# Kernel optimization log

Hardware: AMD Instinct MI355X
Metric: run time of the kernel (lower is better)

The kernel has to match this reference:

```python
import jax, jax.numpy as jnp
import numpy as np

DEMO_T = 4
N_HEADS = 4
N_LAYERS = 2
EPS = 1e-5
IN_DIM = 512
FF_DIM = 128
TEMP = float(np.sqrt(IN_DIM))  # temperature=None -> sqrt(in_dim)


def setup_inputs() -> dict:
    key = jax.random.key(0)
    ks = jax.random.split(key, 12)
    B, d, T, H, W = 8, IN_DIM, 36, 7, 12
    s_in = 1.0 / np.sqrt(d)
    s_ff = 1.0 / np.sqrt(FF_DIM)
    f32 = jnp.float32
    return {
        "inputs": jax.random.normal(ks[0], (B, d, T, H, W), f32),
        "demo_wq": jax.random.normal(ks[1], (N_LAYERS, FF_DIM, d), f32) * s_in,
        "demo_wk": jax.random.normal(ks[2], (N_LAYERS, FF_DIM, d), f32) * s_in,
        "demo_wv": jax.random.normal(ks[3], (N_LAYERS, FF_DIM, d), f32) * s_in,
        "demo_wo": jax.random.normal(ks[4], (N_LAYERS, d, FF_DIM), f32) * s_ff,
        "obs_wq": jax.random.normal(ks[5], (N_LAYERS, FF_DIM, d), f32) * s_in,
        "obs_wk": jax.random.normal(ks[6], (N_LAYERS, FF_DIM, d), f32) * s_in,
        "obs_wv": jax.random.normal(ks[7], (N_LAYERS, FF_DIM, d), f32) * s_in,
        "obs_wo": jax.random.normal(ks[8], (N_LAYERS, d, FF_DIM), f32) * s_ff,
        "bn_gamma": jnp.ones((N_LAYERS, d), f32),
        "bn_beta": jnp.zeros((N_LAYERS, d), f32),
    }


def _conv1x1(w, x):
    # 1x1x1 Conv3d, bias=False == per-voxel channel mixing
    return jnp.einsum('od,bdthw->bothw', w, x)


def _forward(inputs, demo_wq, demo_wk, demo_wv, demo_wo,
             obs_wq, obs_wk, obs_wv, obs_wo, bn_gamma, bn_beta):
    B, d, T, H, W = inputs.shape
    HW = H * W
    obs_T = T - DEMO_T
    neg_inf = jnp.asarray(-jnp.inf, inputs.dtype)
    # causal log-mask over demo tokens, block-expanded to spatial positions
    tril = jnp.tril(jnp.ones((DEMO_T, DEMO_T), inputs.dtype))
    mask = jnp.repeat(jnp.repeat(tril, HW, axis=0), HW, axis=1)  # (dTHW, dTHW)
    log_mask = jnp.where(mask > 0, jnp.asarray(0.0, inputs.dtype), neg_inf)

    x = inputs
    for i in range(N_LAYERS):
        demo_in = x[:, :, :DEMO_T]   # [B,d,dT,H,W]
        obs_in = x[:, :, DEMO_T:]    # [B,d,oT,H,W]

        # --- demo self-attention (causal) ---
        def demo_heads(w):
            y = _conv1x1(w, demo_in)                      # [B,ff,dT,H,W]
            return y.reshape(B, N_HEADS, -1, DEMO_T * HW)  # [B,n,ch,dTHW]
        dq, dk, dv = demo_heads(demo_wq[i]), demo_heads(demo_wk[i]), demo_heads(demo_wv[i])
        dkq = jnp.einsum('bnci,bncj->bnij', dk, dq) / TEMP + log_mask
        dattn = jax.nn.softmax(dkq, axis=-1)               # softmax over j (as in source)
        dv_att = jnp.einsum('bncj,bnij->bnci', dv, dattn)  # attended demo values
        # NOTE: the source computes demo_out via demo_Outs + relu-skip but never
        # uses it downstream (dead code); only dv_att/dk feed the obs fusion.

        # --- obs attention, fused with demo keys/attended-values ---
        def obs_heads(w):
            y = _conv1x1(w, obs_in)                        # [B,ff,oT,H,W]
            y = y.reshape(B, N_HEADS, -1, obs_T, HW)
            return jnp.transpose(y, (0, 3, 1, 2, 4))       # [B,oT,n,ch,HW]
        oq, ok, ov = obs_heads(obs_wq[i]), obs_heads(obs_wk[i]), obs_heads(obs_wv[i])
        rep_k = jnp.broadcast_to(dk[:, None], (B, obs_T) + dk.shape[1:])
        rep_v = jnp.broadcast_to(dv_att[:, None], (B, obs_T) + dv_att.shape[1:])
        cat_k = jnp.concatenate([rep_k, ok], axis=-1)      # [B,oT,n,ch,(1+dT)HW]
        cat_v = jnp.concatenate([rep_v, ov], axis=-1)
        okq = jnp.einsum('btnci,btncj->btnij', cat_k, oq) / TEMP  # i=cat len, j=HW
        oattn = jax.nn.softmax(okq, axis=-1)               # softmax over j (source: dim=4)
        ov_att = jnp.einsum('btncj,btnji->btnci', cat_v, oattn)  # [B,oT,n,ch,HW]
        obs_out = _conv1x1(obs_wo[i],
                           jnp.transpose(ov_att, (0, 2, 3, 1, 4)).reshape(B, -1, obs_T, H, W))
        # skip (out_dim == in_dim), dropout=0 -> identity
        obs_res = obs_in + jax.nn.relu(obs_out)

        # shared BatchNorm3d (training-mode batch stats) over concatenated streams
        x = jnp.concatenate([demo_in, obs_res], axis=2)
        mean = x.mean(axis=(0, 2, 3, 4)).reshape(1, -1, 1, 1, 1)
        var = x.var(axis=(0, 2, 3, 4)).reshape(1, -1, 1, 1, 1)
        g = bn_gamma[i].reshape(1, -1, 1, 1, 1)
        b = bn_beta[i].reshape(1, -1, 1, 1, 1)
        x = g * (x - mean) * jax.lax.rsqrt(var + EPS) + b
    return x  # == out_dict['last']


def reference(inputs, demo_wq, demo_wk, demo_wv, demo_wo,
              obs_wq, obs_wk, obs_wv, obs_wo, bn_gamma, bn_beta):
    return _forward(inputs, demo_wq, demo_wk, demo_wv, demo_wo,
                    obs_wq, obs_wk, obs_wv, obs_wo, bn_gamma, bn_beta)
```

## Files before the change

kernel.cpp:

```cpp
#include <hip/hip_runtime.h>

#define B_N 8
#define D_N 512
#define T_N 36
#define HW_N 84
#define THW_N 3024
#define DT_N 4
#define OT_N 32
#define NH_N 4
#define FF_N 128
#define CH_N 32
#define DI_N 336
#define OI_N 2688
#define CAT_N 420
#define INV_TEMP 0.04419417382415922f
#define BN_EPS 1e-5f
#define INV_CNT (1.0f / 24192.0f)

#define SW_DWQ 0
#define SW_DWK 131072
#define SW_DWV 262144
#define SW_OWQ 393216
#define SW_OWK 524288
#define SW_OWV 655360
#define SW_OWO 786432
#define S_DQ   917504
#define S_DK   1261568
#define S_DV   1605632
#define S_DVA  1949696
#define S_OQ   2293760
#define S_OK   5046272
#define S_OV   7798784
#define S_OVA  10551296
#define S_XBF  13303808

typedef short bf16x8 __attribute__((ext_vector_type(8)));
typedef float f32x4 __attribute__((ext_vector_type(4)));

__device__ __forceinline__ short f2bf(float f) {
    unsigned u = __float_as_uint(f);
    u += 0x7fffu + ((u >> 16) & 1u);
    return (short)(u >> 16);
}
__device__ __forceinline__ float bf2f(short s) {
    return __uint_as_float(((unsigned)(unsigned short)s) << 16);
}

__global__ __launch_bounds__(256) void cvt_w_kernel(
    const float* __restrict__ s0, const float* __restrict__ s1,
    const float* __restrict__ s2, const float* __restrict__ s3,
    const float* __restrict__ s4, const float* __restrict__ s5,
    const float* __restrict__ s6, short* __restrict__ dst,
    float* __restrict__ stats)
{
    const int bid = blockIdx.x;
    if (bid == 0) {
        #pragma unroll
        for (int k = 0; k < 8; ++k) stats[threadIdx.x * 8 + k] = 0.f;
    }
    const int a = bid >> 6, blk = bid & 63;
    const float* src;
    switch (a) {
        case 0: src = s0; break; case 1: src = s1; break;
        case 2: src = s2; break; case 3: src = s3; break;
        case 4: src = s4; break; case 5: src = s5; break;
        default: src = s6;
    }
    const int idx = (blk * 256 + (int)threadIdx.x) * 8;
    float4 f0 = *reinterpret_cast<const float4*>(src + idx);
    float4 f1 = *reinterpret_cast<const float4*>(src + idx + 4);
    bf16x8 pk;
    pk[0] = f2bf(f0.x); pk[1] = f2bf(f0.y); pk[2] = f2bf(f0.z); pk[3] = f2bf(f0.w);
    pk[4] = f2bf(f1.x); pk[5] = f2bf(f1.y); pk[6] = f2bf(f1.z); pk[7] = f2bf(f1.w);
    *reinterpret_cast<bf16x8*>(dst + (size_t)a * 131072 + idx) = pk;
}

__global__ __launch_bounds__(256) void xin_kernel(
    const float* __restrict__ in_f, short* __restrict__ xbf,
    float* __restrict__ stats0)
{
    __shared__ short tile[48][65];
    __shared__ float red_s[16][64];
    __shared__ float red_q[16][64];

    const int bid = blockIdx.x;
    const int b = bid / 504, rem = bid % 504, tt = rem >> 3, cblk = rem & 7;
    const int t0 = tt * 48, c0 = cblk * 64;
    const int tid = threadIdx.x;
    const bool is_demo = (tt < 7);

    #pragma unroll
    for (int l0 = 0; l0 < 768; l0 += 256) {
        int l = l0 + tid;
        int cc = l / 12, tg = l % 12;
        size_t addr = ((size_t)b * D_N + c0 + cc) * THW_N + t0 + tg * 4;
        float4 v = *reinterpret_cast<const float4*>(in_f + addr);
        tile[tg * 4 + 0][cc] = f2bf(v.x);
        tile[tg * 4 + 1][cc] = f2bf(v.y);
        tile[tg * 4 + 2][cc] = f2bf(v.z);
        tile[tg * 4 + 3][cc] = f2bf(v.w);
    }
    __syncthreads();
    float psum[4] = {}, psq[4] = {};
    const int cg = tid & 15;
    #pragma unroll
    for (int l0 = 0; l0 < 768; l0 += 256) {
        int l = l0 + tid;
        int tk = l >> 4;
        short4 s4;
        s4.x = tile[tk][cg * 4 + 0];
        s4.y = tile[tk][cg * 4 + 1];
        s4.z = tile[tk][cg * 4 + 2];
        s4.w = tile[tk][cg * 4 + 3];
        *reinterpret_cast<short4*>(
            xbf + ((size_t)b * THW_N + t0 + tk) * 512 + c0 + cg * 4) = s4;
        if (is_demo) {
            float v0 = bf2f(s4.x), v1 = bf2f(s4.y), v2 = bf2f(s4.z), v3 = bf2f(s4.w);
            psum[0] += v0; psum[1] += v1; psum[2] += v2; psum[3] += v3;
            psq[0] += v0 * v0; psq[1] += v1 * v1; psq[2] += v2 * v2; psq[3] += v3 * v3;
        }
    }
    if (!is_demo) return;
    __syncthreads();
    #pragma unroll
    for (int j = 0; j < 4; ++j) {
        red_s[tid >> 4][cg * 4 + j] = psum[j];
        red_q[tid >> 4][cg * 4 + j] = psq[j];
    }
    __syncthreads();
    if (tid < 64) {
        float s = 0.f, q = 0.f;
        #pragma unroll
        for (int r = 0; r < 16; ++r) { s += red_s[r][tid]; q += red_q[r][tid]; }
        atomicAdd(&stats0[c0 + tid], s);
        atomicAdd(&stats0[512 + c0 + tid], q);
    }
}

__global__ __launch_bounds__(256) void proj_mfma_kernel(
    const short* __restrict__ xbf, short* __restrict__ ws, int layer)
{
    __shared__ short As[3][4096];
    __shared__ short Bs[1536];

    const int bid = blockIdx.x;
    const int b = bid / 63, ct = bid - b * 63;
    const bool is_demo = (ct < 7);
    const int woff = layer * 65536;
    const short* W0 = ws + (is_demo ? SW_DWQ : SW_OWQ) + woff;
    const short* W1 = ws + (is_demo ? SW_DWK : SW_OWK) + woff;
    const short* W2 = ws + (is_demo ? SW_DWV : SW_OWV) + woff;
    const int Ltok = is_demo ? DI_N : OI_N;
    const int colL = is_demo ? ct * 48 : (ct - 7) * 48;
    short* Yq = ws + (is_demo ? S_DQ : S_OQ);
    short* Yk = ws + (is_demo ? S_DK : S_OK);
    short* Yv = ws + (is_demo ? S_DV : S_OV);
    const short* Xb = xbf + ((size_t)b * THW_N + (is_demo ? 0 : DI_N) + colL) * 512;

    const int tid = threadIdx.x;
    const int lane = tid & 63, wv = tid >> 6;
    const int l15 = lane & 15, q = lane >> 4;

    f32x4 acc[3][2][3] = {};

    for (int k0 = 0; k0 < D_N; k0 += 32) {
        __syncthreads();
        const short* Wt[3] = {W0, W1, W2};
        #pragma unroll
        for (int wt = 0; wt < 3; ++wt) {
            #pragma unroll
            for (int h = 0; h < 2; ++h) {
                int c = tid + h * 256;
                int kc = c & 3, m = c >> 2;
                bf16x8 pk = *reinterpret_cast<const bf16x8*>(
                    Wt[wt] + (size_t)m * D_N + k0 + kc * 8);
                *reinterpret_cast<bf16x8*>(&As[wt][(kc * 128 + m) * 8]) = pk;
            }
        }
        if (tid < 192) {
            int n = tid % 48, kc = tid / 48;
            bf16x8 pk = *reinterpret_cast<const bf16x8*>(
                Xb + (size_t)n * 512 + k0 + kc * 8);
            *reinterpret_cast<bf16x8*>(&Bs[(kc * 48 + n) * 8]) = pk;
        }
        __syncthreads();

        bf16x8 bfr[3];
        #pragma unroll
        for (int nt = 0; nt < 3; ++nt)
            bfr[nt] = *reinterpret_cast<const bf16x8*>(&Bs[(q * 48 + nt * 16 + l15) * 8]);
        #pragma unroll
        for (int wt = 0; wt < 3; ++wt) {
            #pragma unroll
            for (int mt2 = 0; mt2 < 2; ++mt2) {
                bf16x8 afr = *reinterpret_cast<const bf16x8*>(
                    &As[wt][(q * 128 + wv * 32 + mt2 * 16 + l15) * 8]);
                #pragma unroll
                for (int nt = 0; nt < 3; ++nt)
                    acc[wt][mt2][nt] = __builtin_amdgcn_mfma_f32_16x16x32_bf16(
                        afr, bfr[nt], acc[wt][mt2][nt], 0, 0, 0);
            }
        }
    }

    #pragma unroll
    for (int mt2 = 0; mt2 < 2; ++mt2) {
        int mrow = wv * 32 + mt2 * 16 + q * 4;
        #pragma unroll
        for (int nt = 0; nt < 3; ++nt) {
            int token = colL + nt * 16 + l15;
            f32x4 aq = acc[0][mt2][nt] * INV_TEMP;
            short4 s4;
            s4.x = f2bf(aq[0]); s4.y = f2bf(aq[1]); s4.z = f2bf(aq[2]); s4.w = f2bf(aq[3]);
            *reinterpret_cast<short4*>(Yq + ((size_t)b * Ltok + token) * 128 + mrow) = s4;
            f32x4 ak = acc[1][mt2][nt];
            s4.x = f2bf(ak[0]); s4.y = f2bf(ak[1]); s4.z = f2bf(ak[2]); s4.w = f2bf(ak[3]);
            *reinterpret_cast<short4*>(Yk + ((size_t)b * Ltok + token) * 128 + mrow) = s4;
            #pragma unroll
            for (int r = 0; r < 4; ++r)
                Yv[((size_t)b * FF_N + mrow + r) * Ltok + token] = f2bf(acc[2][mt2][nt][r]);
        }
    }
}

template<int NT>
__device__ __forceinline__ void demo_core(
    const short* __restrict__ dqS, const short* __restrict__ dkS,
    const short* __restrict__ dvS, short* __restrict__ dvaS,
    short* __restrict__ Pt, int b, int n, int ti, int ih)
{
    constexpr int NTP = (NT + 1) & ~1;
    const int tid = threadIdx.x;
    const int lane = tid & 63, w = tid >> 6;
    const int l15 = lane & 15, q = lane >> 4;
    const int jmax = (ti + 1) * 84;

    const int irow = ih * 48 + w * 16 + l15;
    const int tokA = ti * 84 + (irow < 84 ? irow : 83);
    bf16x8 afr = *reinterpret_cast<const bf16x8*>(
        dkS + ((size_t)b * DI_N + tokA) * 128 + n * 32 + q * 8);

    f32x4 s[NT];
    #pragma unroll
    for (int nt = 0; nt < NT; ++nt) {
        bf16x8 bfr = *reinterpret_cast<const bf16x8*>(
            dqS + ((size_t)b * DI_N + nt * 16 + l15) * 128 + n * 32 + q * 8);
        f32x4 z = {};
        s[nt] = __builtin_amdgcn_mfma_f32_16x16x32_bf16(afr, bfr, z, 0, 0, 0);
    }

    const int mstart = jmax - (NT - 1) * 16;
    #pragma unroll
    for (int r = 0; r < 4; ++r) {
        if (l15 >= mstart) s[NT - 1][r] = -3.0e38f;
        float mx = s[0][r];
        #pragma unroll
        for (int nt = 1; nt < NT; ++nt) mx = fmaxf(mx, s[nt][r]);
        #pragma unroll
        for (int o = 1; o < 16; o <<= 1) mx = fmaxf(mx, __shfl_xor(mx, o));
        float sm = 0.f;
        #pragma unroll
        for (int nt = 0; nt < NT; ++nt) {
            float e = __expf(s[nt][r] - mx);
            s[nt][r] = e; sm += e;
        }
        #pragma unroll
        for (int o = 1; o < 16; o <<= 1) sm += __shfl_xor(sm, o);
        float inv = 1.f / sm;
        #pragma unroll
        for (int nt = 0; nt < NT; ++nt) s[nt][r] *= inv;
    }

    #pragma unroll
    for (int nt = 0; nt < NT; ++nt)
        #pragma unroll
        for (int r = 0; r < 4; ++r)
            Pt[(w * 16 + q * 4 + r) * 360 + nt * 16 + l15] = f2bf(s[nt][r]);
    if (NTP != NT) {
        #pragma unroll
        for (int r = 0; r < 4; ++r)
            Pt[(w * 16 + q * 4 + r) * 360 + NT * 16 + l15] = 0;
    }
    __syncthreads();

    f32x4 oacc[2] = {};
    #pragma unroll
    for (int kk = 0; kk < NTP / 2; ++kk) {
        bf16x8 pb = *reinterpret_cast<const bf16x8*>(
            &Pt[(w * 16 + l15) * 360 + kk * 32 + q * 8]);
        #pragma unroll
        for (int ct = 0; ct < 2; ++ct) {
            bf16x8 va = *reinterpret_cast<const bf16x8*>(
                dvS + ((size_t)b * FF_N + n * 32 + ct * 16 + l15) * DI_N + kk * 32 + q * 8);
            oacc[ct] = __builtin_amdgcn_mfma_f32_16x16x32_bf16(va, pb, oacc[ct], 0, 0, 0);
        }
    }

    const int ig = ih * 48 + w * 16 + l15;
    if (ig < 84) {
        #pragma unroll
        for (int ct = 0; ct < 2; ++ct)
            #pragma unroll
            for (int r = 0; r < 4; ++r)
                dvaS[((size_t)b * FF_N + n * 32 + ct * 16 + q * 4 + r) * DI_N + ti * 84 + ig] =
                    f2bf(oacc[ct][r]);
    }
}

__global__ __launch_bounds__(192) void demo_attn_mfma_kernel(const short* __restrict__ ws)
{
    __shared__ short Pt[48 * 360];

    const short* dqS = ws + S_DQ;
    const short* dkS = ws + S_DK;
    const short* dvS = ws + S_DV;
    short* dvaS = const_cast<short*>(ws) + S_DVA;

    const int bid = blockIdx.x;
    const int ih = bid & 1, ti = (bid >> 1) & 3;
    const int n = (bid >> 3) & 3, b = bid >> 5;

    switch (ti) {
        case 0: demo_core<6>(dqS, dkS, dvS, dvaS, Pt, b, n, ti, ih); break;
        case 1: demo_core<11>(dqS, dkS, dvS, dvaS, Pt, b, n, ti, ih); break;
        case 2: demo_core<16>(dqS, dkS, dvS, dvaS, Pt, b, n, ti, ih); break;
        default: demo_core<21>(dqS, dkS, dvS, dvaS, Pt, b, n, ti, ih); break;
    }
}

__global__ __launch_bounds__(256, 4) void obs_attn_mfma_kernel(const short* __restrict__ ws)
{
    __shared__ short Qt[96 * 40];
    __shared__ short Kt[64 * 40];
    __shared__ short Vs[32 * 72];
    __shared__ short Pt[96 * 72];

    const short* dkS = ws + S_DK;
    const short* dvaS = ws + S_DVA;
    const short* oqS = ws + S_OQ;
    const short* okS = ws + S_OK;
    const short* ovS = ws + S_OV;
    short* ovaS = const_cast<short*>(ws) + S_OVA;

    const int bid = blockIdx.x;
    const int b = bid >> 7, rem = bid & 127, t = rem >> 2, n = rem & 3;

    const int tid = threadIdx.x;
    const int lane = tid & 63, wv = tid >> 6;
    const int l15 = lane & 15, q = lane >> 4;

    for (int l = tid; l < 384; l += 256) {
        int i = l >> 2, c0 = (l & 3) * 8;
        bf16x8 pk = {0,0,0,0,0,0,0,0};
        if (i < HW_N)
            pk = *reinterpret_cast<const bf16x8*>(
                oqS + ((size_t)b * OI_N + t * 84 + i) * 128 + n * 32 + c0);
        *reinterpret_cast<bf16x8*>(&Qt[i * 40 + c0]) = pk;
    }

    const int pv_mt = wv & 1;
    const int pv_nb = wv >> 1;
    f32x4 oacc[3] = {};

    for (int jc = 0; jc < 448; jc += 64) {
        __syncthreads();
        {
            int jl = tid >> 2, c0 = (tid & 3) * 8;
            int jg = jc + jl;
            bf16x8 pk = {0,0,0,0,0,0,0,0};
            if (jg < DI_N)
                pk = *reinterpret_cast<const bf16x8*>(
                    dkS + ((size_t)b * DI_N + jg) * 128 + n * 32 + c0);
            else if (jg < CAT_N)
                pk = *reinterpret_cast<const bf16x8*>(
                    okS + ((size_t)b * OI_N + t * 84 + (jg - DI_N)) * 128 + n * 32 + c0);
            *reinterpret_cast<bf16x8*>(&Kt[jl * 40 + c0]) = pk;
        }
        {
            int c = tid >> 3, j0 = (tid & 7) * 8;
            int jg0 = jc + j0;
            const short* dvaRow = dvaS + ((size_t)b * FF_N + n * 32 + c) * DI_N;
            const short* ovRow = ovS + ((size_t)b * FF_N + n * 32 + c) * OI_N + t * 84;
            bf16x8 pk;
            if (jg0 + 8 <= DI_N) {
                pk = *reinterpret_cast<const bf16x8*>(dvaRow + jg0);
            } else if (jg0 >= DI_N && jg0 + 8 <= CAT_N) {
                short4 lo = *reinterpret_cast<const short4*>(ovRow + (jg0 - DI_N));
                short4 hi = *reinterpret_cast<const short4*>(ovRow + (jg0 - DI_N) + 4);
                pk[0]=lo.x; pk[1]=lo.y; pk[2]=lo.z; pk[3]=lo.w;
                pk[4]=hi.x; pk[5]=hi.y; pk[6]=hi.z; pk[7]=hi.w;
            } else {
                #pragma unroll
                for (int p = 0; p < 8; ++p) {
                    int jg = jg0 + p;
                    pk[p] = (jg < DI_N) ? dvaRow[jg]
                          : ((jg < CAT_N) ? ovRow[jg - DI_N] : (short)0);
                }
            }
            *reinterpret_cast<bf16x8*>(&Vs[c * 72 + j0]) = pk;
        }
        __syncthreads();

        f32x4 s[6];
        bf16x8 afr = *reinterpret_cast<const bf16x8*>(&Kt[(wv * 16 + l15) * 40 + q * 8]);
        #pragma unroll
        for (int nt = 0; nt < 6; ++nt) {
            bf16x8 bfr = *reinterpret_cast<const bf16x8*>(&Qt[(nt * 16 + l15) * 40 + q * 8]);
            f32x4 z = {};
            s[nt] = __builtin_amdgcn_mfma_f32_16x16x32_bf16(afr, bfr, z, 0, 0, 0);
        }
        float inv[4];
        #pragma unroll
        for (int r = 0; r < 4; ++r) {
            if (l15 >= 4) s[5][r] = -3.0e38f;
            float m2 = s[0][r];
            #pragma unroll
            for (int nt2 = 1; nt2 < 6; ++nt2) m2 = fmaxf(m2, s[nt2][r]);
            #pragma unroll
            for (int o = 1; o < 16; o <<= 1) m2 = fmaxf(m2, __shfl_xor(m2, o));
            float sm = 0.f;
            #pragma unroll
            for (int nt2 = 0; nt2 < 6; ++nt2) { float e = __expf(s[nt2][r] - m2); s[nt2][r] = e; sm += e; }
            #pragma unroll
            for (int o = 1; o < 16; o <<= 1) sm += __shfl_xor(sm, o);
            inv[r] = 1.f / sm;
        }
        #pragma unroll
        for (int nt = 0; nt < 6; ++nt) {
            short4 pk4;
            pk4.x = f2bf(s[nt][0] * inv[0]);
            pk4.y = f2bf(s[nt][1] * inv[1]);
            pk4.z = f2bf(s[nt][2] * inv[2]);
            pk4.w = f2bf(s[nt][3] * inv[3]);
            *reinterpret_cast<short4*>(&Pt[(nt * 16 + l15) * 72 + wv * 16 + q * 4]) = pk4;
        }
        __syncthreads();

        #pragma unroll
        for (int kk = 0; kk < 2; ++kk) {
            bf16x8 va = *reinterpret_cast<const bf16x8*>(&Vs[(pv_mt * 16 + l15) * 72 + kk * 32 + q * 8]);
            #pragma unroll
            for (int u = 0; u < 3; ++u) {
                int nt = pv_nb + u * 2;
                bf16x8 pb = *reinterpret_cast<const bf16x8*>(&Pt[(nt * 16 + l15) * 72 + kk * 32 + q * 8]);
                oacc[u] = __builtin_amdgcn_mfma_f32_16x16x32_bf16(va, pb, oacc[u], 0, 0, 0);
            }
        }
    }

    #pragma unroll
    for (int u = 0; u < 3; ++u) {
        int i = (pv_nb + u * 2) * 16 + l15;
        if (i < HW_N) {
            short4 st;
            st.x = f2bf(oacc[u][0]); st.y = f2bf(oacc[u][1]);
            st.z = f2bf(oacc[u][2]); st.w = f2bf(oacc[u][3]);
            *reinterpret_cast<short4*>(
                ovaS + (((size_t)b * OT_N + t) * 84 + i) * 128 + n * 32 + pv_mt * 16 + q * 4) = st;
        }
    }
}

__global__ __launch_bounds__(256) void outproj_mfma_kernel(
    short* __restrict__ xbf, const short* __restrict__ ws, int layer,
    float* __restrict__ stats)
{
    __shared__ short As[4096];
    __shared__ short Bs[3072];

    const int bid = blockIdx.x;
    const int b = bid >> 7, rem = bid & 127, t = rem >> 2, mt = rem & 3;
    const int o0 = mt * 128;
    const short* WoS = ws + SW_OWO + layer * 65536 + (size_t)o0 * FF_N;
    const short* ovaS = ws + S_OVA + (((size_t)b * OT_N + t) * 84) * 128;

    const int tid = threadIdx.x;
    const int lane = tid & 63, wv = tid >> 6;
    const int l15 = lane & 15, q = lane >> 4;

    f32x4 acc[2][6] = {};

    for (int k0 = 0; k0 < FF_N; k0 += 32) {
        __syncthreads();
        #pragma unroll
        for (int h = 0; h < 2; ++h) {
            int c = tid + h * 256;
            int kc = c & 3, m = c >> 2;
            bf16x8 pk = *reinterpret_cast<const bf16x8*>(WoS + (size_t)m * FF_N + k0 + kc * 8);
            *reinterpret_cast<bf16x8*>(&As[(kc * 128 + m) * 8]) = pk;
        }
        for (int c = tid; c < 384; c += 256) {
            int n2 = c % 96, kc = c / 96;
            bf16x8 pk = {0,0,0,0,0,0,0,0};
            if (n2 < HW_N)
                pk = *reinterpret_cast<const bf16x8*>(ovaS + (size_t)n2 * 128 + k0 + kc * 8);
            *reinterpret_cast<bf16x8*>(&Bs[(kc * 96 + n2) * 8]) = pk;
        }
        __syncthreads();

        bf16x8 af[2];
        #pragma unroll
        for (int mt2 = 0; mt2 < 2; ++mt2)
            af[mt2] = *reinterpret_cast<const bf16x8*>(
                &As[(q * 128 + wv * 32 + mt2 * 16 + l15) * 8]);
        #pragma unroll
        for (int nt = 0; nt < 6; ++nt) {
            bf16x8 bf = *reinterpret_cast<const bf16x8*>(&Bs[(q * 96 + nt * 16 + l15) * 8]);
            #pragma unroll
            for (int mt2 = 0; mt2 < 2; ++mt2)
                acc[mt2][nt] = __builtin_amdgcn_mfma_f32_16x16x32_bf16(
                    af[mt2], bf, acc[mt2][nt], 0, 0, 0);
        }
    }

    float csum[2][4] = {}, csq[2][4] = {};
    #pragma unroll
    for (int mt2 = 0; mt2 < 2; ++mt2) {
        const int och = o0 + wv * 32 + mt2 * 16 + q * 4;
        #pragma unroll
        for (int nt = 0; nt < 6; ++nt) {
            int i = nt * 16 + l15;
            if (i < HW_N) {
                short* p = xbf + ((size_t)b * THW_N + (size_t)(DT_N + t) * HW_N + i) * 512 + och;
                short4 old4 = *reinterpret_cast<short4*>(p);
                short4 nw;
                float ov[4] = {bf2f(old4.x), bf2f(old4.y), bf2f(old4.z), bf2f(old4.w)};
                short* nwp = &nw.x;
                #pragma unroll
                for (int r = 0; r < 4; ++r) {
                    float v = acc[mt2][nt][r];
                    float y = ov[r] + (v > 0.f ? v : 0.f);
                    short ybf = f2bf(y);
                    nwp[r] = ybf;
                    float yr = bf2f(ybf);
                    csum[mt2][r] += yr;
                    csq[mt2][r] += yr * yr;
                }
                *reinterpret_cast<short4*>(p) = nw;
            }
        }
    }
    #pragma unroll
    for (int mt2 = 0; mt2 < 2; ++mt2) {
        #pragma unroll
        for (int r = 0; r < 4; ++r) {
            float s = csum[mt2][r], qq = csq[mt2][r];
            #pragma unroll
            for (int o = 1; o < 16; o <<= 1) {
                s += __shfl_xor(s, o);
                qq += __shfl_xor(qq, o);
            }
            if (l15 == 0) {
                int ch = o0 + wv * 32 + mt2 * 16 + q * 4 + r;
                atomicAdd(&stats[ch], s);
                atomicAdd(&stats[512 + ch], qq);
            }
        }
    }
}

__global__ __launch_bounds__(256) void bn_mid_kernel(
    short* __restrict__ xbf, const float* __restrict__ stats,
    const float* __restrict__ gamma, const float* __restrict__ beta,
    float* __restrict__ stats_next)
{
    __shared__ float red_s[4][512];
    __shared__ float red_q[4][512];

    const int bid = blockIdx.x;
    const int b = bid / 63, tt = bid % 63;
    const int t0 = tt * 48;
    const bool is_demo = (tt < 7);
    const int tid = threadIdx.x;
    const int chg = tid & 63;
    const int trow = tid >> 6;

    float mean[8], rs[8], g[8], bb[8];
    #pragma unroll
    for (int j = 0; j < 8; ++j) {
        int c = chg * 8 + j;
        float m = stats[c] * INV_CNT;
        float var = stats[512 + c] * INV_CNT - m * m;
        mean[j] = m;
        rs[j] = rsqrtf(var + BN_EPS);
        g[j] = gamma[c];
        bb[j] = beta[c];
    }

    float psum[8] = {}, psq[8] = {};
    #pragma unroll
    for (int it = 0; it < 12; ++it) {
        int tok = t0 + it * 4 + trow;
        short* p = xbf + ((size_t)b * THW_N + tok) * 512 + chg * 8;
        bf16x8 v = *reinterpret_cast<bf16x8*>(p);
        bf16x8 w;
        #pragma unroll
        for (int j = 0; j < 8; ++j) {
            float y = g[j] * (bf2f(v[j]) - mean[j]) * rs[j] + bb[j];
            short yb = f2bf(y);
            w[j] = yb;
            if (is_demo) {
                float yr = bf2f(yb);
                psum[j] += yr; psq[j] += yr * yr;
            }
        }
        *reinterpret_cast<bf16x8*>(p) = w;
    }
    if (!is_demo) return;
    #pragma unroll
    for (int j = 0; j < 8; ++j) {
        red_s[trow][chg * 8 + j] = psum[j];
        red_q[trow][chg * 8 + j] = psq[j];
    }
    __syncthreads();
    #pragma unroll
    for (int h = 0; h < 2; ++h) {
        int c = tid + h * 256;
        float s = red_s[0][c] + red_s[1][c] + red_s[2][c] + red_s[3][c];
        float qq = red_q[0][c] + red_q[1][c] + red_q[2][c] + red_q[3][c];
        atomicAdd(&stats_next[c], s);
        atomicAdd(&stats_next[512 + c], qq);
    }
}

__global__ __launch_bounds__(256) void bn_out_kernel(
    const short* __restrict__ xbf, float* __restrict__ out_f,
    const float* __restrict__ stats,
    const float* __restrict__ gamma, const float* __restrict__ beta)
{
    __shared__ float tile[48][65];

    const int bid = blockIdx.x;
    const int b = bid / 504, rem = bid % 504, tt = rem >> 3, cblk = rem & 7;
    const int t0 = tt * 48, c0 = cblk * 64;
    const int tid = threadIdx.x;
    const int cg = tid & 15;

    float mean[4], rs[4], g[4], bb[4];
    #pragma unroll
    for (int j = 0; j < 4; ++j) {
        int c = c0 + cg * 4 + j;
        float m = stats[c] * INV_CNT;
        float var = stats[512 + c] * INV_CNT - m * m;
        mean[j] = m; rs[j] = rsqrtf(var + BN_EPS);
        g[j] = gamma[c]; bb[j] = beta[c];
    }

    #pragma unroll
    for (int l0 = 0; l0 < 768; l0 += 256) {
        int l = l0 + tid;
        int tok = l >> 4;
        short4 v = *reinterpret_cast<const short4*>(
            xbf + ((size_t)b * THW_N + t0 + tok) * 512 + c0 + cg * 4);
        tile[tok][cg * 4 + 0] = g[0] * (bf2f(v.x) - mean[0]) * rs[0] + bb[0];
        tile[tok][cg * 4 + 1] = g[1] * (bf2f(v.y) - mean[1]) * rs[1] + bb[1];
        tile[tok][cg * 4 + 2] = g[2] * (bf2f(v.z) - mean[2]) * rs[2] + bb[2];
        tile[tok][cg * 4 + 3] = g[3] * (bf2f(v.w) - mean[3]) * rs[3] + bb[3];
    }
    __syncthreads();
    #pragma unroll
    for (int l0 = 0; l0 < 768; l0 += 256) {
        int l = l0 + tid;
        int cc = l / 12, tg = l % 12;
        float4 o;
        o.x = tile[tg * 4 + 0][cc];
        o.y = tile[tg * 4 + 1][cc];
        o.z = tile[tg * 4 + 2][cc];
        o.w = tile[tg * 4 + 3][cc];
        *reinterpret_cast<float4*>(
            out_f + ((size_t)b * D_N + c0 + cc) * THW_N + t0 + tg * 4) = o;
    }
}

extern "C" void kernel_launch(void* const* d_in, const int* in_sizes, int n_in,
                              void* d_out, int out_size, void* d_ws, size_t ws_size,
                              hipStream_t stream)
{
    const float* inp  = (const float*)d_in[0];
    const float* dwq  = (const float*)d_in[1];
    const float* dwk  = (const float*)d_in[2];
    const float* dwv  = (const float*)d_in[3];
    const float* owq  = (const float*)d_in[5];
    const float* owk  = (const float*)d_in[6];
    const float* owv  = (const float*)d_in[7];
    const float* owo  = (const float*)d_in[8];
    const float* gam  = (const float*)d_in[9];
    const float* bet  = (const float*)d_in[10];
    float* x  = (float*)d_out;
    float* stats = (float*)d_ws;
    short* wsS = (short*)(stats + 2048);
    short* xbf = wsS + S_XBF;

    cvt_w_kernel<<<448, 256, 0, stream>>>(dwq, dwk, dwv, owq, owk, owv, owo, wsS, stats);
    xin_kernel<<<4032, 256, 0, stream>>>(inp, xbf, stats);

    for (int layer = 0; layer < 2; ++layer) {
        float* stL = stats + layer * 1024;
        size_t coff = (size_t)layer * D_N;
        proj_mfma_kernel<<<504, 256, 0, stream>>>(xbf, wsS, layer);
        demo_attn_mfma_kernel<<<256, 192, 0, stream>>>(wsS);
        obs_attn_mfma_kernel<<<1024, 256, 0, stream>>>(wsS);
        outproj_mfma_kernel<<<1024, 256, 0, stream>>>(xbf, wsS, layer, stL);
        if (layer == 0) {
            bn_mid_kernel<<<504, 256, 0, stream>>>(
                xbf, stL, gam + coff, bet + coff, stats + 1024);
        } else {
            bn_out_kernel<<<4032, 256, 0, stream>>>(
                xbf, x, stL, gam + coff, bet + coff);
        }
    }
    (void)in_sizes; (void)n_in; (void)out_size; (void)ws_size;
}
```

Before: 350.0 us.

## Retile obs output projection to register-resident fragments without LDS staging

```diff
diff --git a/kernel.cpp b/kernel.cpp
--- a/kernel.cpp
+++ b/kernel.cpp
@@ -465,97 +465,97 @@
     short* __restrict__ xbf, const short* __restrict__ ws, int layer,
     float* __restrict__ stats)
 {
-    __shared__ short As[4096];
-    __shared__ short Bs[3072];
+    __shared__ float redS[4][32];
+    __shared__ float redQ[4][32];
 
     const int bid = blockIdx.x;
-    const int b = bid >> 7, rem = bid & 127, t = rem >> 2, mt = rem & 3;
-    const int o0 = mt * 128;
-    const short* WoS = ws + SW_OWO + layer * 65536 + (size_t)o0 * FF_N;
-    const short* ovaS = ws + S_OVA + (((size_t)b * OT_N + t) * 84) * 128;
+    const int t8 = bid & 7;
+    const int rr = bid >> 3;
+    const int c32 = rr & 15;
+    const int tc = rr >> 4;
+    const int tchunk = tc * 8 + t8;
+    const int o0 = c32 * 32;
 
     const int tid = threadIdx.x;
     const int lane = tid & 63, wv = tid >> 6;
     const int l15 = lane & 15, q = lane >> 4;
 
-    f32x4 acc[2][6] = {};
-
-    for (int k0 = 0; k0 < FF_N; k0 += 32) {
-        __syncthreads();
-        #pragma unroll
-        for (int h = 0; h < 2; ++h) {
-            int c = tid + h * 256;
-            int kc = c & 3, m = c >> 2;
-            bf16x8 pk = *reinterpret_cast<const bf16x8*>(WoS + (size_t)m * FF_N + k0 + kc * 8);
-            *reinterpret_cast<bf16x8*>(&As[(kc * 128 + m) * 8]) = pk;
-        }
-        for (int c = tid; c < 384; c += 256) {
-            int n2 = c % 96, kc = c / 96;
-            bf16x8 pk = {0,0,0,0,0,0,0,0};
-            if (n2 < HW_N)
-                pk = *reinterpret_cast<const bf16x8*>(ovaS + (size_t)n2 * 128 + k0 + kc * 8);
-            *reinterpret_cast<bf16x8*>(&Bs[(kc * 96 + n2) * 8]) = pk;
-        }
-        __syncthreads();
-
-        bf16x8 af[2];
-        #pragma unroll
-        for (int mt2 = 0; mt2 < 2; ++mt2)
-            af[mt2] = *reinterpret_cast<const bf16x8*>(
-                &As[(q * 128 + wv * 32 + mt2 * 16 + l15) * 8]);
-        #pragma unroll
-        for (int nt = 0; nt < 6; ++nt) {
-            bf16x8 bf = *reinterpret_cast<const bf16x8*>(&Bs[(q * 96 + nt * 16 + l15) * 8]);
-            #pragma unroll
-            for (int mt2 = 0; mt2 < 2; ++mt2)
-                acc[mt2][nt] = __builtin_amdgcn_mfma_f32_16x16x32_bf16(
-                    af[mt2], bf, acc[mt2][nt], 0, 0, 0);
-        }
-    }
+    const int g0 = tchunk * 192 + wv * 48;
+    const int b = g0 / OI_N;
+    const size_t xbase = (size_t)(g0 + DI_N * (b + 1)) * 512 + o0;
+
+    const short* Wo = ws + SW_OWO + layer * 65536;
+    const short* ova = ws + S_OVA;
+
+    bf16x8 afr[2][4];
+    #pragma unroll
+    for (int mt = 0; mt < 2; ++mt)
+        #pragma unroll
+        for (int kc = 0; kc < 4; ++kc)
+            afr[mt][kc] = *reinterpret_cast<const bf16x8*>(
+                Wo + (size_t)(o0 + mt * 16 + l15) * FF_N + kc * 32 + q * 8);
 
     float csum[2][4] = {}, csq[2][4] = {};
-    #pragma unroll
-    for (int mt2 = 0; mt2 < 2; ++mt2) {
-        const int och = o0 + wv * 32 + mt2 * 16 + q * 4;
-        #pragma unroll
-        for (int nt = 0; nt < 6; ++nt) {
-            int i = nt * 16 + l15;
-            if (i < HW_N) {
-                short* p = xbf + ((size_t)b * THW_N + (size_t)(DT_N + t) * HW_N + i) * 512 + och;
-                short4 old4 = *reinterpret_cast<short4*>(p);
-                short4 nw;
-                float ov[4] = {bf2f(old4.x), bf2f(old4.y), bf2f(old4.z), bf2f(old4.w)};
-                short* nwp = &nw.x;
-                #pragma unroll
-                for (int r = 0; r < 4; ++r) {
-                    float v = acc[mt2][nt][r];
-                    float y = ov[r] + (v > 0.f ? v : 0.f);
-                    short ybf = f2bf(y);
-                    nwp[r] = ybf;
-                    float yr = bf2f(ybf);
-                    csum[mt2][r] += yr;
-                    csq[mt2][r] += yr * yr;
-                }
-                *reinterpret_cast<short4*>(p) = nw;
+
+    #pragma unroll
+    for (int nt = 0; nt < 3; ++nt) {
+        const int g = g0 + nt * 16;
+        const short* ovaT = ova + (size_t)(g + l15) * FF_N + q * 8;
+        bf16x8 bfr[4];
+        #pragma unroll
+        for (int kc = 0; kc < 4; ++kc)
+            bfr[kc] = *reinterpret_cast<const bf16x8*>(ovaT + kc * 32);
+
+        f32x4 acc[2] = {};
+        #pragma unroll
+        for (int kc = 0; kc < 4; ++kc) {
+            acc[0] = __builtin_amdgcn_mfma_f32_16x16x32_bf16(afr[0][kc], bfr[kc], acc[0], 0, 0, 0);
+            acc[1] = __builtin_amdgcn_mfma_f32_16x16x32_bf16(afr[1][kc], bfr[kc], acc[1], 0, 0, 0);
+        }
+
+        #pragma unroll
+        for (int mt = 0; mt < 2; ++mt) {
+            short* p = xbf + xbase + (size_t)(nt * 16 + l15) * 512 + mt * 16 + q * 4;
+            short4 old4 = *reinterpret_cast<short4*>(p);
+            float ov[4] = {bf2f(old4.x), bf2f(old4.y), bf2f(old4.z), bf2f(old4.w)};
+            short4 nw;
+            short* nwp = &nw.x;
+            #pragma unroll
+            for (int r = 0; r < 4; ++r) {
+                float v = acc[mt][r];
+                float y = ov[r] + (v > 0.f ? v : 0.f);
+                short ybf = f2bf(y);
+                nwp[r] = ybf;
+                float yr = bf2f(ybf);
+                csum[mt][r] += yr;
+                csq[mt][r] += yr * yr;
             }
-        }
-    }
-    #pragma unroll
-    for (int mt2 = 0; mt2 < 2; ++mt2) {
+            *reinterpret_cast<short4*>(p) = nw;
+        }
+    }
+
+    #pragma unroll
+    for (int mt = 0; mt < 2; ++mt) {
         #pragma unroll
         for (int r = 0; r < 4; ++r) {
-            float s = csum[mt2][r], qq = csq[mt2][r];
+            float s = csum[mt][r], qq = csq[mt][r];
             #pragma unroll
             for (int o = 1; o < 16; o <<= 1) {
                 s += __shfl_xor(s, o);
                 qq += __shfl_xor(qq, o);
             }
             if (l15 == 0) {
-                int ch = o0 + wv * 32 + mt2 * 16 + q * 4 + r;
-                atomicAdd(&stats[ch], s);
-                atomicAdd(&stats[512 + ch], qq);
+                redS[wv][mt * 16 + q * 4 + r] = s;
+                redQ[wv][mt * 16 + q * 4 + r] = qq;
             }
         }
+    }
+    __syncthreads();
+    if (tid < 32) {
+        float s = redS[0][tid] + redS[1][tid] + redS[2][tid] + redS[3][tid];
+        float qq = redQ[0][tid] + redQ[1][tid] + redQ[2][tid] + redQ[3][tid];
+        atomicAdd(&stats[o0 + tid], s);
+        atomicAdd(&stats[512 + o0 + tid], qq);
     }
 }
 
@@ -700,7 +700,7 @@
         proj_mfma_kernel<<<504, 256, 0, stream>>>(xbf, wsS, layer);
         demo_attn_mfma_kernel<<<256, 192, 0, stream>>>(wsS);
         obs_attn_mfma_kernel<<<1024, 256, 0, stream>>>(wsS);
-        outproj_mfma_kernel<<<1024, 256, 0, stream>>>(xbf, wsS, layer, stL);
+        outproj_mfma_kernel<<<1792, 256, 0, stream>>>(xbf, wsS, layer, stL);
         if (layer == 0) {
             bn_mid_kernel<<<504, 256, 0, stream>>>(
                 xbf, stL, gam + coff, bet + coff, stats + 1024);
```

Result: faster. 321.6 us (-8.1%).
